# Kernel optimization log

Measured on AMD Instinct MI355X. Metric: run time of the kernel, lower is better.

The kernel has to match this reference:

```python
import jax, jax.numpy as jnp
import numpy as np
from jax import lax

N = 2048
B = 64
T = 128
INPUT_DIM = 4
OUTPUT_DIM = 2
N_SENS = 256
N_OUT = 128


def setup_inputs() -> dict:
    key = jax.random.key(0)
    ks = jax.random.split(key, 6)
    inputs = jax.random.normal(ks[0], (B, T, INPUT_DIM), dtype=jnp.float32)
    # scale recurrent weights so repeated relu(h@W) does not blow up
    W_rec = jax.random.normal(ks[1], (N, N), dtype=jnp.float32) * (0.9 / np.sqrt(N))
    scale_in = 1.0 / np.sqrt(INPUT_DIM)
    scale_out = 1.0 / np.sqrt(N_OUT)
    W_in = jax.random.uniform(ks[2], (N_SENS, INPUT_DIM), dtype=jnp.float32,
                              minval=-scale_in, maxval=scale_in)
    b_in = jnp.zeros((N_SENS,), dtype=jnp.float32)
    W_out = jax.random.uniform(ks[3], (OUTPUT_DIM, N_OUT), dtype=jnp.float32,
                               minval=-scale_out, maxval=scale_out)
    b_out = jnp.zeros((OUTPUT_DIM,), dtype=jnp.float32)
    sensory_indices = jax.random.permutation(ks[4], N)[:N_SENS].astype(jnp.int64)
    output_indices = jax.random.permutation(ks[5], N)[:N_OUT].astype(jnp.int64)
    return {"inputs": inputs, "W_rec": W_rec, "W_in": W_in, "b_in": b_in,
            "W_out": W_out, "b_out": b_out,
            "sensory_indices": sensory_indices, "output_indices": output_indices,
            "K": 4}


def reference(inputs, W_rec, W_in, b_in, W_out, b_out,
              sensory_indices, output_indices, K):
    # inputs: [B, T, I]; h: [B, N]
    rec_t = W_rec.T  # h @ W_rec.T as in torch code
    batch = inputs.shape[0]
    h0 = jnp.zeros((batch, W_rec.shape[0]), dtype=inputs.dtype)

    def micro(h, _):
        return jax.nn.relu(h @ rec_t), None

    def timestep(h, x_t):  # x_t: [B, I]
        injection = x_t @ W_in.T + b_in               # [B, n_sens]
        next_h = (h @ rec_t).at[:, sensory_indices].add(injection)
        h = jax.nn.relu(next_h)                       # microstep 0
        h, _ = lax.scan(micro, h, None, length=K - 1) # remaining microsteps
        readout = h[:, output_indices] @ W_out.T + b_out  # [B, OUTPUT_DIM]
        return h, readout

    _, outs = lax.scan(timestep, h0, jnp.swapaxes(inputs, 0, 1))  # [T, B, O]
    return jnp.swapaxes(outs, 0, 1)  # [B, T, O]
```

## Files before the change

kernel.cpp:

```cpp
#include <hip/hip_runtime.h>


#define N_DIM   2048
#define B_DIM   64
#define T_DIM   128
#define NSENS   256
#define NOUT    128
#define NSTEP   512

#define NWG     256
#define THREADS 512
#define CW      32
#define RING    3
#define SLOT_F16 (B_DIM * N_DIM)
#define SP_S    20
#define SP_HALF (256 * SP_S)
#define LDS_W_F16 (CW * N_DIM)
#define SMEM_MAIN (LDS_W_F16 * 2 + 2 * SP_HALF * 2)

typedef _Float16 f16x8 __attribute__((ext_vector_type(8)));
typedef _Float16 f16x4 __attribute__((ext_vector_type(4)));
typedef float    f32x4 __attribute__((ext_vector_type(4)));
typedef unsigned long long u64;
typedef unsigned short u16;

#define SIGN_M32 0x80008000u
#define SIGN_M64 0x8000800080008000ULL

union V16 { uint4 q; u64 u[2]; };


__global__ void k_init(uint4* __restrict__ ring, int* __restrict__ inv_sens,
                       int* __restrict__ inv_out, u64* __restrict__ flags) {
    const int i = blockIdx.x * blockDim.x + threadIdx.x;
    const int slot = i / (SLOT_F16 / 8);
    if (slot < RING) {
        const unsigned pat = (slot == 0 || (slot & 1)) ? SIGN_M32 : 0u;
        ring[i] = make_uint4(pat, pat, pat, pat);
    }
    if (i < N_DIM) { inv_sens[i] = -1; inv_out[i] = -1; }
    if (i < 64) flags[i] = 0ull;
}

__global__ void k_inv_scatter(int* inv_sens, int* inv_out,
                              const int* sidx, const int* oidx) {
    int i = threadIdx.x;
    if (i < NSENS) inv_sens[sidx[i]] = i;
    if (i < NOUT)  inv_out[oidx[i]] = i;
}


__global__ __launch_bounds__(THREADS, 2)
void rnn_main(const float* __restrict__ W_rec, const float* __restrict__ inputs,
              const float* __restrict__ W_in, const float* __restrict__ b_in,
              const int* __restrict__ inv_sens, const int* __restrict__ inv_out,
              _Float16* __restrict__ ring, _Float16* __restrict__ hc,
              u16* __restrict__ flags )
{
    extern __shared__ _Float16 smem[];
    _Float16* w_hi = smem;
    _Float16* sp   = smem + LDS_W_F16;

    const int tid   = threadIdx.x;
    const int wg    = blockIdx.x;
    const int pl    = wg & 3;
    const int cg    = wg >> 2;
    const int jbase = cg * CW;

    const int lane = tid & 63;
    const int wv   = tid >> 6;
    const int lrow = lane & 15;
    const int quad = lane >> 4;
    (void)flags;

    f16x8 blo[8][2];
#pragma unroll
    for (int nt = 0; nt < 2; ++nt) {
        const float* wr = W_rec + (size_t)(jbase + nt * 16 + lrow) * N_DIM
                        + wv * 256 + quad * 8;
#pragma unroll
        for (int ks = 0; ks < 8; ++ks) {
            const float4 wa = ((const float4*)(wr + ks * 32))[0];
            const float4 wb = ((const float4*)(wr + ks * 32))[1];
            const float w8[8] = {wa.x, wa.y, wa.z, wa.w, wb.x, wb.y, wb.z, wb.w};
            f16x8 hi8;
#pragma unroll
            for (int e = 0; e < 8; ++e) {
                const _Float16 hi = (_Float16)w8[e];
                hi8[e] = hi;
                blo[ks][nt][e] = (_Float16)((w8[e] - (float)hi) * 4096.0f);
            }
            *(f16x8*)(w_hi + ((((wv * 8 + ks) * 2 + nt)) << 9) + lane * 8) = hi8;
        }
    }

    const int ep_bl = tid >> 4;
    const int ep_b  = pl * 16 + ep_bl;
    const int ep_jp = tid & 15;
    const int ej    = jbase + ep_jp * 2;
    int ep_sA = -1, ep_sB = -1, ep_uA = -1, ep_uB = -1, ep_off = 0;
    if (tid < 256) {
        ep_sA = inv_sens[ej];  ep_sB = inv_sens[ej + 1];
        ep_uA = inv_out[ej];   ep_uB = inv_out[ej + 1];
        ep_off = ((pl * 64 + cg) << 9)
               + ((((ej >> 3) & 3) * 16 + ep_bl) << 3) + (ej & 7);
    }
    __syncthreads();

    int slot_r = 0, slot_w = 1;

    for (int step = 0; step < NSTEP; ++step) {
        const int t = step >> 2, micro = step & 3;
        const bool expSet = (step & 1) == 0;
        const _Float16* __restrict__ hcur = ring + (size_t)slot_r * SLOT_F16;
        _Float16* __restrict__       hnxt = ring + (size_t)slot_w * SLOT_F16;

        f16x8 bh[8][2];
#pragma unroll
        for (int ks = 0; ks < 8; ++ks)
#pragma unroll
            for (int nt = 0; nt < 2; ++nt)
                bh[ks][nt] = *(const f16x8*)(w_hi + (((wv * 8 + ks) * 2 + nt) << 9) + lane * 8);

        const _Float16* hb = hcur + ((pl * 64 + wv * 8) << 9) + lane * 8;
        V16 a[8];
        asm volatile(
            "global_load_dwordx4 %0, %8, off sc1\n\t"
            "global_load_dwordx4 %1, %9, off sc1\n\t"
            "global_load_dwordx4 %2, %10, off sc1\n\t"
            "global_load_dwordx4 %3, %11, off sc1\n\t"
            "global_load_dwordx4 %4, %12, off sc1\n\t"
            "global_load_dwordx4 %5, %13, off sc1\n\t"
            "global_load_dwordx4 %6, %14, off sc1\n\t"
            "global_load_dwordx4 %7, %15, off sc1\n\t"
            "s_waitcnt vmcnt(0)"
            : "=v"(a[0].q), "=v"(a[1].q), "=v"(a[2].q), "=v"(a[3].q),
              "=v"(a[4].q), "=v"(a[5].q), "=v"(a[6].q), "=v"(a[7].q)
            : "v"(hb),        "v"(hb + 512),  "v"(hb + 1024), "v"(hb + 1536),
              "v"(hb + 2048), "v"(hb + 2560), "v"(hb + 3072), "v"(hb + 3584)
            : "memory");

        f32x4 acch[2], accl[2];
#pragma unroll
        for (int nt = 0; nt < 2; ++nt) {
            acch[nt] = (f32x4){0.f, 0.f, 0.f, 0.f};
            accl[nt] = (f32x4){0.f, 0.f, 0.f, 0.f};
        }

        unsigned live = 0xFFu;
        while (live) {
#pragma unroll
            for (int f = 0; f < 8; ++f) if (live & (1u << f)) {
                const u64 band = a[f].u[0] & a[f].u[1];
                const u64 bor  = a[f].u[0] | a[f].u[1];
                const bool ok = expSet ? ((band & SIGN_M64) == SIGN_M64)
                                       : ((bor  & SIGN_M64) == 0);
                if (__all((int)ok)) {
                    union { u64 u[2]; f16x8 v; } c;
                    c.u[0] = expSet ? (a[f].u[0] ^ SIGN_M64) : a[f].u[0];
                    c.u[1] = expSet ? (a[f].u[1] ^ SIGN_M64) : a[f].u[1];
                    const f16x8 Af = c.v;
                    acch[0] = __builtin_amdgcn_mfma_f32_16x16x32_f16(Af, bh[f][0], acch[0], 0, 0, 0);
                    accl[0] = __builtin_amdgcn_mfma_f32_16x16x32_f16(Af, blo[f][0], accl[0], 0, 0, 0);
                    acch[1] = __builtin_amdgcn_mfma_f32_16x16x32_f16(Af, bh[f][1], acch[1], 0, 0, 0);
                    accl[1] = __builtin_amdgcn_mfma_f32_16x16x32_f16(Af, blo[f][1], accl[1], 0, 0, 0);
                    live &= ~(1u << f);
                }
            }
            if (live) {
                __builtin_amdgcn_s_sleep(1);
#pragma unroll
                for (int f = 0; f < 8; ++f) if (live & (1u << f))
                    asm volatile("global_load_dwordx4 %0, %1, off sc1"
                                 : "=v"(a[f].q) : "v"(hb + f * 512) : "memory");
                asm volatile("s_waitcnt vmcnt(0)" ::: "memory");
                __builtin_amdgcn_sched_barrier(0);
            }
        }

        _Float16* sph = sp + (step & 1) * SP_HALF;
#pragma unroll
        for (int nt = 0; nt < 2; ++nt) {
            f16x4 pv;
#pragma unroll
            for (int r = 0; r < 4; ++r)
                pv[r] = (_Float16)(acch[nt][r] + accl[nt][r] * 2.44140625e-4f);
            *(f16x4*)(sph + (wv * 32 + nt * 16 + lrow) * SP_S + quad * 4) = pv;
        }
        __syncthreads();

        if (tid < 256) {
            float vA = 0.f, vB = 0.f;
#pragma unroll
            for (int s8 = 0; s8 < 8; ++s8) {
                vA += (float)sph[(s8 * 32 + ep_jp * 2    ) * SP_S + ep_bl];
                vB += (float)sph[(s8 * 32 + ep_jp * 2 + 1) * SP_S + ep_bl];
            }
            if (micro == 0 && (ep_sA >= 0 || ep_sB >= 0)) {
                const float4 x = *(const float4*)(inputs + ((ep_b * T_DIM + t) << 2));
                if (ep_sA >= 0) {
                    const float4 w = *(const float4*)(W_in + (ep_sA << 2));
                    vA += b_in[ep_sA] + x.x * w.x + x.y * w.y + x.z * w.z + x.w * w.w;
                }
                if (ep_sB >= 0) {
                    const float4 w = *(const float4*)(W_in + (ep_sB << 2));
                    vB += b_in[ep_sB] + x.x * w.x + x.y * w.y + x.z * w.z + x.w * w.w;
                }
            }
            union { _Float16 h[2]; unsigned u; } pk;
            pk.h[0] = (_Float16)fmaxf(vA, 0.0f);
            pk.h[1] = (_Float16)fmaxf(vB, 0.0f);
            if (micro == 3) {
                if (ep_uA >= 0) hc[(t * NOUT + ep_uA) * B_DIM + ep_b] = pk.h[0];
                if (ep_uB >= 0) hc[(t * NOUT + ep_uB) * B_DIM + ep_b] = pk.h[1];
            }
            pk.u |= (step & 1) ? SIGN_M32 : 0u;
            __hip_atomic_store((unsigned*)(hnxt + ep_off), pk.u,
                               __ATOMIC_RELAXED, __HIP_MEMORY_SCOPE_AGENT);
        }
        __syncthreads();

        slot_r = (slot_r + 1 == RING) ? 0 : slot_r + 1;
        slot_w = (slot_w + 1 == RING) ? 0 : slot_w + 1;
    }
}


__global__ __launch_bounds__(128)
void k_readout(float* __restrict__ out, const _Float16* __restrict__ hc,
               const float* __restrict__ W_out, const float* __restrict__ b_out) {
    __shared__ _Float16 sh[NOUT * B_DIM];
    const int t = blockIdx.x, tid = threadIdx.x;
    const unsigned int* src = (const unsigned int*)(hc + (size_t)t * NOUT * B_DIM);
    for (int i = tid; i < NOUT * B_DIM / 2; i += 128)
        ((unsigned int*)sh)[i] = src[i];
    __syncthreads();
    const int o = tid >> 6, b = tid & 63;
    float acc = b_out[o];
#pragma unroll 8
    for (int u = 0; u < NOUT; ++u)
        acc += (float)sh[u * B_DIM + b] * W_out[o * NOUT + u];
    out[(b * T_DIM + t) * 2 + o] = acc;
}


extern "C" void kernel_launch(void* const* d_in, const int* in_sizes, int n_in,
                              void* d_out, int out_size, void* d_ws, size_t ws_size,
                              hipStream_t stream) {
    const float* inputs = (const float*)d_in[0];
    const float* W_rec  = (const float*)d_in[1];
    const float* W_in   = (const float*)d_in[2];
    const float* b_in   = (const float*)d_in[3];
    const float* W_out  = (const float*)d_in[4];
    const float* b_out  = (const float*)d_in[5];
    const int*   sidx   = (const int*)d_in[6];
    const int*   oidx   = (const int*)d_in[7];

    char* ws = (char*)d_ws;
    _Float16* ring     = (_Float16*)ws;
    _Float16* hc       = (_Float16*)(ws + 786432);
    int*      inv_sens = (int*)(ws + 786432 + 2097152);
    int*      inv_out  = inv_sens + N_DIM;
    u16*      flags    = (u16*)(inv_out + N_DIM);

    k_init<<<192, 256, 0, stream>>>((uint4*)ring, inv_sens, inv_out, (u64*)flags);
    k_inv_scatter<<<1, 256, 0, stream>>>(inv_sens, inv_out, sidx, oidx);

    (void)hipFuncSetAttribute((const void*)rnn_main,
                              hipFuncAttributeMaxDynamicSharedMemorySize, SMEM_MAIN);

    rnn_main<<<NWG, THREADS, SMEM_MAIN, stream>>>(
        W_rec, inputs, W_in, b_in, inv_sens, inv_out, ring, hc, flags);

    k_readout<<<T_DIM, 128, 0, stream>>>((float*)d_out, hc, W_out, b_out);
}
```

Baseline: 1.531 ms.

## Pipeline per-fragment state polling and spread epilogue reduction across all waves

The per-step state loads are now consumed one fragment at a time with staggered vmcnt waits, so each fragment's MFMAs start as soon as its data arrives instead of after all eight loads finish. The LDS weight reads are issued after the global loads to overlap their latency. The epilogue reduction is split across all 512 threads, with each half-wave summing four partials and combining them by shuffle. The trailing __syncthreads is dropped, which relies on double-buffered LDS partials to stay safe. The readiness-flag protocol and the retry loop are kept, with the retry restructured around the initial per-fragment pass.

```diff
diff --git a/kernel.cpp b/kernel.cpp
--- a/kernel.cpp
+++ b/kernel.cpp
@@ -50,6 +50,25 @@
 }
 
 
+#define CONSUME(F, VM) do {                                                   \
+    asm volatile("s_waitcnt vmcnt(" #VM ")" ::: "memory");                    \
+    __builtin_amdgcn_sched_barrier(0);                                        \
+    const u64 band = a[F].u[0] & a[F].u[1];                                   \
+    const u64 bor  = a[F].u[0] | a[F].u[1];                                   \
+    const bool ok = expSet ? ((band & SIGN_M64) == SIGN_M64)                  \
+                           : ((bor  & SIGN_M64) == 0);                        \
+    if (__all((int)ok)) {                                                     \
+        union { u64 u[2]; f16x8 v; } c;                                       \
+        c.u[0] = expSet ? (a[F].u[0] ^ SIGN_M64) : a[F].u[0];                 \
+        c.u[1] = expSet ? (a[F].u[1] ^ SIGN_M64) : a[F].u[1];                 \
+        const f16x8 Af = c.v;                                                 \
+        acch[0] = __builtin_amdgcn_mfma_f32_16x16x32_f16(Af, bh[F][0], acch[0], 0, 0, 0); \
+        accl[0] = __builtin_amdgcn_mfma_f32_16x16x32_f16(Af, blo[F][0], accl[0], 0, 0, 0); \
+        acch[1] = __builtin_amdgcn_mfma_f32_16x16x32_f16(Af, bh[F][1], acch[1], 0, 0, 0); \
+        accl[1] = __builtin_amdgcn_mfma_f32_16x16x32_f16(Af, blo[F][1], accl[1], 0, 0, 0); \
+    } else live |= (1u << F);                                                 \
+} while (0)
+
 __global__ __launch_bounds__(THREADS, 2)
 void rnn_main(const float* __restrict__ W_rec, const float* __restrict__ inputs,
               const float* __restrict__ W_in, const float* __restrict__ b_in,
@@ -94,17 +113,16 @@
         }
     }
 
-    const int ep_bl = tid >> 4;
-    const int ep_b  = pl * 16 + ep_bl;
-    const int ep_jp = tid & 15;
-    const int ej    = jbase + ep_jp * 2;
-    int ep_sA = -1, ep_sB = -1, ep_uA = -1, ep_uB = -1, ep_off = 0;
-    if (tid < 256) {
-        ep_sA = inv_sens[ej];  ep_sB = inv_sens[ej + 1];
-        ep_uA = inv_out[ej];   ep_uB = inv_out[ej + 1];
-        ep_off = ((pl * 64 + cg) << 9)
-               + ((((ej >> 3) & 3) * 16 + ep_bl) << 3) + (ej & 7);
-    }
+    const int eo    = wv * 32 + (lane & 31);
+    const int ebl   = eo >> 4;
+    const int ejp   = eo & 15;
+    const int ehalf = lane >> 5;
+    const int ep_b  = pl * 16 + ebl;
+    const int ej    = jbase + ejp * 2;
+    const int ep_sA = inv_sens[ej], ep_sB = inv_sens[ej + 1];
+    const int ep_uA = inv_out[ej],  ep_uB = inv_out[ej + 1];
+    const int ep_off = ((pl * 64 + cg) << 9)
+                     + ((((ej >> 3) & 3) * 16 + ebl) << 3) + (ej & 7);
     __syncthreads();
 
     int slot_r = 0, slot_w = 1;
@@ -114,13 +132,6 @@
         const bool expSet = (step & 1) == 0;
         const _Float16* __restrict__ hcur = ring + (size_t)slot_r * SLOT_F16;
         _Float16* __restrict__       hnxt = ring + (size_t)slot_w * SLOT_F16;
-
-        f16x8 bh[8][2];
-#pragma unroll
-        for (int ks = 0; ks < 8; ++ks)
-#pragma unroll
-            for (int nt = 0; nt < 2; ++nt)
-                bh[ks][nt] = *(const f16x8*)(w_hi + (((wv * 8 + ks) * 2 + nt) << 9) + lane * 8);
 
         const _Float16* hb = hcur + ((pl * 64 + wv * 8) << 9) + lane * 8;
         V16 a[8];
@@ -132,14 +143,20 @@
             "global_load_dwordx4 %4, %12, off sc1\n\t"
             "global_load_dwordx4 %5, %13, off sc1\n\t"
             "global_load_dwordx4 %6, %14, off sc1\n\t"
-            "global_load_dwordx4 %7, %15, off sc1\n\t"
-            "s_waitcnt vmcnt(0)"
+            "global_load_dwordx4 %7, %15, off sc1"
             : "=v"(a[0].q), "=v"(a[1].q), "=v"(a[2].q), "=v"(a[3].q),
               "=v"(a[4].q), "=v"(a[5].q), "=v"(a[6].q), "=v"(a[7].q)
             : "v"(hb),        "v"(hb + 512),  "v"(hb + 1024), "v"(hb + 1536),
               "v"(hb + 2048), "v"(hb + 2560), "v"(hb + 3072), "v"(hb + 3584)
             : "memory");
 
+        f16x8 bh[8][2];
+#pragma unroll
+        for (int ks = 0; ks < 8; ++ks)
+#pragma unroll
+            for (int nt = 0; nt < 2; ++nt)
+                bh[ks][nt] = *(const f16x8*)(w_hi + (((wv * 8 + ks) * 2 + nt) << 9) + lane * 8);
+
         f32x4 acch[2], accl[2];
 #pragma unroll
         for (int nt = 0; nt < 2; ++nt) {
@@ -147,8 +164,18 @@
             accl[nt] = (f32x4){0.f, 0.f, 0.f, 0.f};
         }
 
-        unsigned live = 0xFFu;
+        unsigned live = 0u;
+        CONSUME(0, 7); CONSUME(1, 6); CONSUME(2, 5); CONSUME(3, 4);
+        CONSUME(4, 3); CONSUME(5, 2); CONSUME(6, 1); CONSUME(7, 0);
+
         while (live) {
+            __builtin_amdgcn_s_sleep(1);
+#pragma unroll
+            for (int f = 0; f < 8; ++f) if (live & (1u << f))
+                asm volatile("global_load_dwordx4 %0, %1, off sc1"
+                             : "=v"(a[f].q) : "v"(hb + f * 512) : "memory");
+            asm volatile("s_waitcnt vmcnt(0)" ::: "memory");
+            __builtin_amdgcn_sched_barrier(0);
 #pragma unroll
             for (int f = 0; f < 8; ++f) if (live & (1u << f)) {
                 const u64 band = a[f].u[0] & a[f].u[1];
@@ -167,15 +194,6 @@
                     live &= ~(1u << f);
                 }
             }
-            if (live) {
-                __builtin_amdgcn_s_sleep(1);
-#pragma unroll
-                for (int f = 0; f < 8; ++f) if (live & (1u << f))
-                    asm volatile("global_load_dwordx4 %0, %1, off sc1"
-                                 : "=v"(a[f].q) : "v"(hb + f * 512) : "memory");
-                asm volatile("s_waitcnt vmcnt(0)" ::: "memory");
-                __builtin_amdgcn_sched_barrier(0);
-            }
         }
 
         _Float16* sph = sp + (step & 1) * SP_HALF;
@@ -189,36 +207,40 @@
         }
         __syncthreads();
 
-        if (tid < 256) {
+        {
             float vA = 0.f, vB = 0.f;
 #pragma unroll
-            for (int s8 = 0; s8 < 8; ++s8) {
-                vA += (float)sph[(s8 * 32 + ep_jp * 2    ) * SP_S + ep_bl];
-                vB += (float)sph[(s8 * 32 + ep_jp * 2 + 1) * SP_S + ep_bl];
-            }
-            if (micro == 0 && (ep_sA >= 0 || ep_sB >= 0)) {
-                const float4 x = *(const float4*)(inputs + ((ep_b * T_DIM + t) << 2));
-                if (ep_sA >= 0) {
-                    const float4 w = *(const float4*)(W_in + (ep_sA << 2));
-                    vA += b_in[ep_sA] + x.x * w.x + x.y * w.y + x.z * w.z + x.w * w.w;
+            for (int s = 0; s < 4; ++s) {
+                const int s8 = ehalf * 4 + s;
+                vA += (float)sph[(s8 * 32 + ejp * 2    ) * SP_S + ebl];
+                vB += (float)sph[(s8 * 32 + ejp * 2 + 1) * SP_S + ebl];
+            }
+            vA += __shfl_xor(vA, 32, 64);
+            vB += __shfl_xor(vB, 32, 64);
+            if (lane < 32) {
+                if (micro == 0 && (ep_sA >= 0 || ep_sB >= 0)) {
+                    const float4 x = *(const float4*)(inputs + ((ep_b * T_DIM + t) << 2));
+                    if (ep_sA >= 0) {
+                        const float4 w = *(const float4*)(W_in + (ep_sA << 2));
+                        vA += b_in[ep_sA] + x.x * w.x + x.y * w.y + x.z * w.z + x.w * w.w;
+                    }
+                    if (ep_sB >= 0) {
+                        const float4 w = *(const float4*)(W_in + (ep_sB << 2));
+                        vB += b_in[ep_sB] + x.x * w.x + x.y * w.y + x.z * w.z + x.w * w.w;
+                    }
                 }
-                if (ep_sB >= 0) {
-                    const float4 w = *(const float4*)(W_in + (ep_sB << 2));
-                    vB += b_in[ep_sB] + x.x * w.x + x.y * w.y + x.z * w.z + x.w * w.w;
+                union { _Float16 h[2]; unsigned u; } pk;
+                pk.h[0] = (_Float16)fmaxf(vA, 0.0f);
+                pk.h[1] = (_Float16)fmaxf(vB, 0.0f);
+                const unsigned pr = pk.u | ((step & 1) ? SIGN_M32 : 0u);
+                __hip_atomic_store((unsigned*)(hnxt + ep_off), pr,
+                                   __ATOMIC_RELAXED, __HIP_MEMORY_SCOPE_AGENT);
+                if (micro == 3) {
+                    if (ep_uA >= 0) hc[(t * NOUT + ep_uA) * B_DIM + ep_b] = pk.h[0];
+                    if (ep_uB >= 0) hc[(t * NOUT + ep_uB) * B_DIM + ep_b] = pk.h[1];
                 }
             }
-            union { _Float16 h[2]; unsigned u; } pk;
-            pk.h[0] = (_Float16)fmaxf(vA, 0.0f);
-            pk.h[1] = (_Float16)fmaxf(vB, 0.0f);
-            if (micro == 3) {
-                if (ep_uA >= 0) hc[(t * NOUT + ep_uA) * B_DIM + ep_b] = pk.h[0];
-                if (ep_uB >= 0) hc[(t * NOUT + ep_uB) * B_DIM + ep_b] = pk.h[1];
-            }
-            pk.u |= (step & 1) ? SIGN_M32 : 0u;
-            __hip_atomic_store((unsigned*)(hnxt + ep_off), pk.u,
-                               __ATOMIC_RELAXED, __HIP_MEMORY_SCOPE_AGENT);
-        }
-        __syncthreads();
+        }
 
         slot_r = (slot_r + 1 == RING) ? 0 : slot_r + 1;
         slot_w = (slot_w + 1 == RING) ? 0 : slot_w + 1;
```

New measurement: 2.919 ms. 1.91x slower.

## Halve workgroup count, double columns per workgroup, fold lo-weight MFMAs into one accumulator

Applied to the files above, without the earlier changes.

Each workgroup now owns 64 output columns instead of 32, so the persistent grid shrinks from 256 to 128 workgroups at one workgroup per CU. High-part weights are split between LDS (read inside the MFMA loop) and registers, and the low-part correction is folded into the same accumulator by pre-scaling A in fp16. The change also issues the state loads before zeroing the accumulators, sleeps only after a few polling rounds, and publishes the state before writing the readout. Fewer workgroups means fewer participants in the grid-wide flag sync and less redundant state reading. The costs are more register pressure, twice the MFMA work per workgroup, and some precision loss from scaling A in fp16.

```diff
diff --git a/kernel.cpp b/kernel.cpp
--- a/kernel.cpp
+++ b/kernel.cpp
@@ -8,15 +8,15 @@
 #define NOUT    128
 #define NSTEP   512
 
-#define NWG     256
+#define NWG     128
 #define THREADS 512
-#define CW      32
+#define CW      64
 #define RING    3
 #define SLOT_F16 (B_DIM * N_DIM)
 #define SP_S    20
-#define SP_HALF (256 * SP_S)
-#define LDS_W_F16 (CW * N_DIM)
-#define SMEM_MAIN (LDS_W_F16 * 2 + 2 * SP_HALF * 2)
+#define SP_ROWS 512
+#define LDS_W_F16 (32 * N_DIM)
+#define SMEM_MAIN (LDS_W_F16 * 2 + SP_ROWS * SP_S * 2)
 
 typedef _Float16 f16x8 __attribute__((ext_vector_type(8)));
 typedef _Float16 f16x4 __attribute__((ext_vector_type(4)));
@@ -50,7 +50,7 @@
 }
 
 
-__global__ __launch_bounds__(THREADS, 2)
+__global__ __launch_bounds__(THREADS, 1)
 void rnn_main(const float* __restrict__ W_rec, const float* __restrict__ inputs,
               const float* __restrict__ W_in, const float* __restrict__ b_in,
               const int* __restrict__ inv_sens, const int* __restrict__ inv_out,
@@ -73,9 +73,10 @@
     const int quad = lane >> 4;
     (void)flags;
 
-    f16x8 blo[8][2];
-#pragma unroll
-    for (int nt = 0; nt < 2; ++nt) {
+    f16x8 blo[8][4];
+    f16x8 bh23[8][2];
+#pragma unroll
+    for (int nt = 0; nt < 4; ++nt) {
         const float* wr = W_rec + (size_t)(jbase + nt * 16 + lrow) * N_DIM
                         + wv * 256 + quad * 8;
 #pragma unroll
@@ -90,21 +91,23 @@
                 hi8[e] = hi;
                 blo[ks][nt][e] = (_Float16)((w8[e] - (float)hi) * 4096.0f);
             }
-            *(f16x8*)(w_hi + ((((wv * 8 + ks) * 2 + nt)) << 9) + lane * 8) = hi8;
+            if (nt < 2)
+                *(f16x8*)(w_hi + ((((wv * 8 + ks) * 2 + nt)) << 9) + lane * 8) = hi8;
+            else
+                bh23[ks][nt - 2] = hi8;
         }
     }
 
-    const int ep_bl = tid >> 4;
-    const int ep_b  = pl * 16 + ep_bl;
-    const int ep_jp = tid & 15;
-    const int ej    = jbase + ep_jp * 2;
-    int ep_sA = -1, ep_sB = -1, ep_uA = -1, ep_uB = -1, ep_off = 0;
-    if (tid < 256) {
-        ep_sA = inv_sens[ej];  ep_sB = inv_sens[ej + 1];
-        ep_uA = inv_out[ej];   ep_uB = inv_out[ej + 1];
-        ep_off = ((pl * 64 + cg) << 9)
-               + ((((ej >> 3) & 3) * 16 + ep_bl) << 3) + (ej & 7);
-    }
+    const int d    = tid;
+    const int r    = d & 255;
+    const int frag = d >> 8;
+    const int ebl  = (r >> 2) & 15;
+    const int jl   = frag * 32 + ((r >> 6) & 3) * 8 + (r & 3) * 2;
+    const int ep_b = pl * 16 + ebl;
+    const int ej   = jbase + jl;
+    const int ep_sA = inv_sens[ej], ep_sB = inv_sens[ej + 1];
+    const int ep_uA = inv_out[ej],  ep_uB = inv_out[ej + 1];
+    const int ep_off = ((pl * 64 + 2 * cg) << 9) + (d << 1);
     __syncthreads();
 
     int slot_r = 0, slot_w = 1;
@@ -114,13 +117,6 @@
         const bool expSet = (step & 1) == 0;
         const _Float16* __restrict__ hcur = ring + (size_t)slot_r * SLOT_F16;
         _Float16* __restrict__       hnxt = ring + (size_t)slot_w * SLOT_F16;
-
-        f16x8 bh[8][2];
-#pragma unroll
-        for (int ks = 0; ks < 8; ++ks)
-#pragma unroll
-            for (int nt = 0; nt < 2; ++nt)
-                bh[ks][nt] = *(const f16x8*)(w_hi + (((wv * 8 + ks) * 2 + nt) << 9) + lane * 8);
 
         const _Float16* hb = hcur + ((pl * 64 + wv * 8) << 9) + lane * 8;
         V16 a[8];
@@ -132,22 +128,22 @@
             "global_load_dwordx4 %4, %12, off sc1\n\t"
             "global_load_dwordx4 %5, %13, off sc1\n\t"
             "global_load_dwordx4 %6, %14, off sc1\n\t"
-            "global_load_dwordx4 %7, %15, off sc1\n\t"
-            "s_waitcnt vmcnt(0)"
+            "global_load_dwordx4 %7, %15, off sc1"
             : "=v"(a[0].q), "=v"(a[1].q), "=v"(a[2].q), "=v"(a[3].q),
               "=v"(a[4].q), "=v"(a[5].q), "=v"(a[6].q), "=v"(a[7].q)
             : "v"(hb),        "v"(hb + 512),  "v"(hb + 1024), "v"(hb + 1536),
               "v"(hb + 2048), "v"(hb + 2560), "v"(hb + 3072), "v"(hb + 3584)
             : "memory");
 
-        f32x4 acch[2], accl[2];
-#pragma unroll
-        for (int nt = 0; nt < 2; ++nt) {
-            acch[nt] = (f32x4){0.f, 0.f, 0.f, 0.f};
-            accl[nt] = (f32x4){0.f, 0.f, 0.f, 0.f};
-        }
+        f32x4 acc[4];
+#pragma unroll
+        for (int nt = 0; nt < 4; ++nt) acc[nt] = (f32x4){0.f, 0.f, 0.f, 0.f};
+
+        asm volatile("s_waitcnt vmcnt(0)" ::: "memory");
+        __builtin_amdgcn_sched_barrier(0);
 
         unsigned live = 0xFFu;
+        int rounds = 0;
         while (live) {
 #pragma unroll
             for (int f = 0; f < 8; ++f) if (live & (1u << f)) {
@@ -160,15 +156,25 @@
                     c.u[0] = expSet ? (a[f].u[0] ^ SIGN_M64) : a[f].u[0];
                     c.u[1] = expSet ? (a[f].u[1] ^ SIGN_M64) : a[f].u[1];
                     const f16x8 Af = c.v;
-                    acch[0] = __builtin_amdgcn_mfma_f32_16x16x32_f16(Af, bh[f][0], acch[0], 0, 0, 0);
-                    accl[0] = __builtin_amdgcn_mfma_f32_16x16x32_f16(Af, blo[f][0], accl[0], 0, 0, 0);
-                    acch[1] = __builtin_amdgcn_mfma_f32_16x16x32_f16(Af, bh[f][1], acch[1], 0, 0, 0);
-                    accl[1] = __builtin_amdgcn_mfma_f32_16x16x32_f16(Af, blo[f][1], accl[1], 0, 0, 0);
+                    f16x8 Al;
+#pragma unroll
+                    for (int e = 0; e < 8; ++e)
+                        Al[e] = Af[e] * (_Float16)2.44140625e-4f;
+                    const f16x8 b0 = *(const f16x8*)(w_hi + (((wv * 8 + f) * 2 + 0) << 9) + lane * 8);
+                    const f16x8 b1 = *(const f16x8*)(w_hi + (((wv * 8 + f) * 2 + 1) << 9) + lane * 8);
+                    acc[0] = __builtin_amdgcn_mfma_f32_16x16x32_f16(Af, b0, acc[0], 0, 0, 0);
+                    acc[0] = __builtin_amdgcn_mfma_f32_16x16x32_f16(Al, blo[f][0], acc[0], 0, 0, 0);
+                    acc[1] = __builtin_amdgcn_mfma_f32_16x16x32_f16(Af, b1, acc[1], 0, 0, 0);
+                    acc[1] = __builtin_amdgcn_mfma_f32_16x16x32_f16(Al, blo[f][1], acc[1], 0, 0, 0);
+                    acc[2] = __builtin_amdgcn_mfma_f32_16x16x32_f16(Af, bh23[f][0], acc[2], 0, 0, 0);
+                    acc[2] = __builtin_amdgcn_mfma_f32_16x16x32_f16(Al, blo[f][2], acc[2], 0, 0, 0);
+                    acc[3] = __builtin_amdgcn_mfma_f32_16x16x32_f16(Af, bh23[f][1], acc[3], 0, 0, 0);
+                    acc[3] = __builtin_amdgcn_mfma_f32_16x16x32_f16(Al, blo[f][3], acc[3], 0, 0, 0);
                     live &= ~(1u << f);
                 }
             }
             if (live) {
-                __builtin_amdgcn_s_sleep(1);
+                if (++rounds >= 3) __builtin_amdgcn_s_sleep(1);
 #pragma unroll
                 for (int f = 0; f < 8; ++f) if (live & (1u << f))
                     asm volatile("global_load_dwordx4 %0, %1, off sc1"
@@ -178,23 +184,22 @@
             }
         }
 
-        _Float16* sph = sp + (step & 1) * SP_HALF;
-#pragma unroll
-        for (int nt = 0; nt < 2; ++nt) {
+#pragma unroll
+        for (int nt = 0; nt < 4; ++nt) {
             f16x4 pv;
 #pragma unroll
-            for (int r = 0; r < 4; ++r)
-                pv[r] = (_Float16)(acch[nt][r] + accl[nt][r] * 2.44140625e-4f);
-            *(f16x4*)(sph + (wv * 32 + nt * 16 + lrow) * SP_S + quad * 4) = pv;
+            for (int rr = 0; rr < 4; ++rr)
+                pv[rr] = (_Float16)acc[nt][rr];
+            *(f16x4*)(sp + (wv * 64 + nt * 16 + lrow) * SP_S + quad * 4) = pv;
         }
         __syncthreads();
 
-        if (tid < 256) {
+        {
             float vA = 0.f, vB = 0.f;
 #pragma unroll
             for (int s8 = 0; s8 < 8; ++s8) {
-                vA += (float)sph[(s8 * 32 + ep_jp * 2    ) * SP_S + ep_bl];
-                vB += (float)sph[(s8 * 32 + ep_jp * 2 + 1) * SP_S + ep_bl];
+                vA += (float)sp[(s8 * 64 + jl    ) * SP_S + ebl];
+                vB += (float)sp[(s8 * 64 + jl + 1) * SP_S + ebl];
             }
             if (micro == 0 && (ep_sA >= 0 || ep_sB >= 0)) {
                 const float4 x = *(const float4*)(inputs + ((ep_b * T_DIM + t) << 2));
@@ -210,13 +215,13 @@
             union { _Float16 h[2]; unsigned u; } pk;
             pk.h[0] = (_Float16)fmaxf(vA, 0.0f);
             pk.h[1] = (_Float16)fmaxf(vB, 0.0f);
+            const unsigned pr = pk.u | ((step & 1) ? SIGN_M32 : 0u);
+            __hip_atomic_store((unsigned*)(hnxt + ep_off), pr,
+                               __ATOMIC_RELAXED, __HIP_MEMORY_SCOPE_AGENT);
             if (micro == 3) {
                 if (ep_uA >= 0) hc[(t * NOUT + ep_uA) * B_DIM + ep_b] = pk.h[0];
                 if (ep_uB >= 0) hc[(t * NOUT + ep_uB) * B_DIM + ep_b] = pk.h[1];
             }
-            pk.u |= (step & 1) ? SIGN_M32 : 0u;
-            __hip_atomic_store((unsigned*)(hnxt + ep_off), pk.u,
-                               __ATOMIC_RELAXED, __HIP_MEMORY_SCOPE_AGENT);
         }
         __syncthreads();
 
```

After: 2.273 ms. 1.48x slower.
